# Optimization experiments

Measured on AMD Instinct MI355X. Metric: run time of the kernel, lower is better.

Reference implementation:

```python
import jax, jax.numpy as jnp
import numpy as np
import math

DIM = 1024
MAX_DEPTH = 16
ROPE_BASE = 10000.0
NUM_ACTIVE = 2

def setup_inputs() -> dict:
    key = jax.random.key(0)
    ks = jax.random.split(key, 6)
    bsz, seq, dim, E, hidden = 4, 1024, DIM, 8, 4 * DIM
    bound = 1.0 / math.sqrt(dim)
    return {
        "x": jax.random.normal(ks[0], (bsz, seq, dim), jnp.float32),
        "router_w": jax.random.normal(ks[1], (dim, dim), jnp.float32) * 0.02,
        "expert_keys": jax.random.uniform(ks[2], (E, dim), jnp.float32, -bound, bound),
        "expert_bias": jnp.zeros((E,), jnp.float32),
        "fc_w": jax.random.normal(ks[3], (E, hidden, dim), jnp.float32) * 0.02,
        "proj_w": jax.random.normal(ks[4], (E, dim, hidden), jnp.float32) * 0.02,
        "depth_idx": 3,
    }

def _rope_row(depth_idx, rev_idx, dtype):
    half = DIM // 2
    inv_freq = 1.0 / (ROPE_BASE ** (jnp.arange(0, DIM, 2, dtype=jnp.float32) / DIM))  # [half]
    f = depth_idx * inv_freq
    r = rev_idx * inv_freq
    return (jnp.cos(f).astype(dtype), jnp.sin(f).astype(dtype),
            jnp.cos(r).astype(dtype), jnp.sin(r).astype(dtype))

def reference(x, router_w, expert_keys, expert_bias, fc_w, proj_w, depth_idx):
    bsz, seq, dim = x.shape
    N = bsz * seq
    flat_x = x.reshape(N, dim)
    # router + RMSNorm (no weight, eps = machine eps, matching F.rms_norm default)
    q = flat_x @ router_w.T
    eps = jnp.asarray(jnp.finfo(q.dtype).eps, q.dtype)
    q = q * jax.lax.rsqrt(jnp.mean(q * q, axis=-1, keepdims=True) + eps)
    # depth RoPE (forward freq on first half pairing, reverse freq on second half)
    half = dim // 2
    cos, sin, rcos, rsin = _rope_row(float(depth_idx), float(MAX_DEPTH - 1 - depth_idx), q.dtype)
    q1, q2 = q[..., :half], q[..., half:]
    q = jnp.concatenate((q1 * cos + q2 * sin, -q1 * rsin + q2 * rcos), axis=-1)
    # routing
    logits = (q @ expert_keys.T) / math.sqrt(dim)  # [N, E]
    gate_values = jax.nn.sigmoid(logits)
    biased = logits + expert_bias
    _, topk_idx = jax.lax.top_k(biased, NUM_ACTIVE)  # [N, k]
    topk_gates = jnp.take_along_axis(gate_values, topk_idx, axis=-1)
    topk_gates = topk_gates / jnp.clip(topk_gates.sum(-1, keepdims=True), 1e-9, None)
    gates = jnp.zeros_like(gate_values).at[jnp.arange(N)[:, None], topk_idx].set(topk_gates)
    # dense all-expert MLP: relu(x W_fc^T)^2 W_proj^T, then mask-and-sum
    h = jax.nn.relu(jnp.einsum('nd,ehd->neh', flat_x, fc_w))
    expert_out = jnp.einsum('neh,edh->ned', h * h, proj_w)  # [N, E, dim]
    y = jnp.einsum('ned,ne->nd', expert_out, gates)
    return y.reshape(bsz, seq, dim)
```

## Files before the change

kernel.cpp:

```cpp
#include <hip/hip_runtime.h>
#include <hip/hip_bf16.h>
#include <math.h>

#define N_TOK 4096
#define DIM_V 1024
#define NEXP  8
#define HID   4096
#define NSLOT 9216

typedef short  s16x8 __attribute__((ext_vector_type(8)));
typedef unsigned short u16x8 __attribute__((ext_vector_type(8)));
typedef unsigned short u16x4 __attribute__((ext_vector_type(4)));
typedef float  f32x4 __attribute__((ext_vector_type(4)));

constexpr size_t OFF_XB   = 0;
constexpr size_t OFF_WB   = OFF_XB + 8388608;
constexpr size_t OFF_RK   = OFF_WB + 2097152;
constexpr size_t OFF_KPP  = OFF_RK + 65536;
constexpr size_t OFF_SSQ  = OFF_KPP + 65536;
constexpr size_t OFF_CNT  = OFF_SSQ + 16384;
constexpr size_t OFF_CUR  = OFF_CNT + 128;
constexpr size_t OFF_TOK  = OFF_CUR + 128;
constexpr size_t OFF_GSL  = OFF_TOK + 36864;
constexpr size_t ZERO_BEG = OFF_KPP;
constexpr size_t ZERO_END = OFF_GSL + 36864;
constexpr size_t OFF_OFFP = ZERO_END;
constexpr size_t OFF_IDX2 = OFF_OFFP + 128;
constexpr size_t OFF_G2   = OFF_IDX2 + 32768;
constexpr size_t OFF_INV  = OFF_G2 + 32768;
constexpr size_t SMALL_END = OFF_INV + 32768;

constexpr size_t A_OFF_FCB = SMALL_END;
constexpr size_t A_OFF_PO  = A_OFF_FCB;
constexpr size_t A_OFF_PJB = A_OFF_FCB + 67108864;
constexpr size_t A_OFF_H2  = A_OFF_PJB + 67108864;
constexpr size_t WS_FULL   = A_OFF_H2 + 75497472;

__device__ inline unsigned short f2bf(float f) {
  __hip_bfloat16 h = __float2bfloat16(f);
  return __builtin_bit_cast(unsigned short, h);
}

__device__ __forceinline__ void gload16(const void* g, void* l) {
  __builtin_amdgcn_global_load_lds(
      (const __attribute__((address_space(1))) unsigned int*)g,
      (__attribute__((address_space(3))) unsigned int*)l, 16, 0, 0);
}

__global__ __launch_bounds__(256) void k_cvt_all(
    const float* __restrict__ x, const float* __restrict__ rw,
    const float* __restrict__ fw, const float* __restrict__ pw,
    unsigned short* __restrict__ xb, unsigned short* __restrict__ wb,
    unsigned short* __restrict__ fcb, unsigned short* __restrict__ pjb) {
  constexpr int NX4 = (N_TOK * DIM_V) / 4;
  constexpr int NW4 = (DIM_V * DIM_V) / 4;
  constexpr int NF4 = (NEXP * HID * DIM_V) / 4;
  constexpr int NU  = (NX4 + NW4 + 2 * NF4) / 1024;
  const int upb = (NU + (int)gridDim.x - 1) / (int)gridDim.x;
  for (int k = 0; k < upb; ++k) {
    int u = (int)blockIdx.x * upb + k;
    if (u >= NU) break;
    int f4 = u * 1024;
    const float4* s; unsigned short* d; int base;
    if (f4 < NX4)                   { s = (const float4*)x;  d = xb;  base = f4; }
    else if (f4 < NX4 + NW4)        { s = (const float4*)rw; d = wb;  base = f4 - NX4; }
    else if (f4 < NX4 + NW4 + NF4)  { s = (const float4*)fw; d = fcb; base = f4 - NX4 - NW4; }
    else                            { s = (const float4*)pw; d = pjb; base = f4 - NX4 - NW4 - NF4; }
    int j = base + (int)threadIdx.x;
    const f32x4* s4 = (const f32x4*)s;
    f32x4 v0 = __builtin_nontemporal_load(s4 + j);
    f32x4 v1 = __builtin_nontemporal_load(s4 + j + 256);
    f32x4 v2 = __builtin_nontemporal_load(s4 + j + 512);
    f32x4 v3 = __builtin_nontemporal_load(s4 + j + 768);
    u16x4 o0 = { f2bf(v0.x), f2bf(v0.y), f2bf(v0.z), f2bf(v0.w) };
    u16x4 o1 = { f2bf(v1.x), f2bf(v1.y), f2bf(v1.z), f2bf(v1.w) };
    u16x4 o2 = { f2bf(v2.x), f2bf(v2.y), f2bf(v2.z), f2bf(v2.w) };
    u16x4 o3 = { f2bf(v3.x), f2bf(v3.y), f2bf(v3.z), f2bf(v3.w) };
    __builtin_nontemporal_store(o0, (u16x4*)(d + (size_t)j * 4));
    __builtin_nontemporal_store(o1, (u16x4*)(d + (size_t)(j + 256) * 4));
    __builtin_nontemporal_store(o2, (u16x4*)(d + (size_t)(j + 512) * 4));
    __builtin_nontemporal_store(o3, (u16x4*)(d + (size_t)(j + 768) * 4));
  }
}

__global__ void k_ropekeys(const float* __restrict__ keys, const int* __restrict__ depth,
                           double* __restrict__ rk) {
  int i = threadIdx.x;
  if (i >= 512) return;
  int dep = depth[0];
  double p = pow(10000.0, (double)i / 512.0);
  float invf = 1.0f / (float)p;
  float ff = (float)dep * invf;
  float rr = (float)(15 - dep) * invf;
  float cf  = (float)cos((double)ff);
  float sf  = (float)sin((double)ff);
  float rcf = (float)cos((double)rr);
  float rsf = (float)sin((double)rr);
  for (int e = 0; e < NEXP; ++e) {
    double k1 = (double)keys[e * DIM_V + i];
    double k2 = (double)keys[e * DIM_V + 512 + i];
    rk[e * DIM_V + i]       = (double)cf  * k1 - (double)rsf * k2;
    rk[e * DIM_V + 512 + i] = (double)sf  * k1 + (double)rcf * k2;
  }
}

__global__ __launch_bounds__(256) void k_colsum(const float* __restrict__ W,
                                                const double* __restrict__ rk,
                                                double* __restrict__ kpp) {
  int j  = blockIdx.x * 256 + threadIdx.x;
  int d0 = blockIdx.y * 64;
  double acc[NEXP] = {};
  for (int dd = 0; dd < 64; ++dd) {
    int d = d0 + dd;
    double w = (double)W[(size_t)d * DIM_V + j];
#pragma unroll
    for (int e = 0; e < NEXP; ++e) acc[e] += w * rk[e * DIM_V + d];
  }
  for (int e = 0; e < NEXP; ++e) atomicAdd(&kpp[e * DIM_V + j], acc[e]);
}

__global__ __launch_bounds__(256) void k_gate(const float* __restrict__ x,
                                              const double* __restrict__ kpp,
                                              const float* __restrict__ sumsq,
                                              const float* __restrict__ bias,
                                              int* __restrict__ idx2, float* __restrict__ gates2,
                                              int* __restrict__ counts) {
  int wave = (blockIdx.x * 256 + threadIdx.x) >> 6;
  int lane = threadIdx.x & 63;
  if (wave >= N_TOK) return;
  const float4* xr = (const float4*)(x + (size_t)wave * DIM_V);
  double a[NEXP] = {};
#pragma unroll
  for (int j = 0; j < 4; ++j) {
    int c = lane + 64 * j;
    float4 v = xr[c];
#pragma unroll
    for (int e = 0; e < NEXP; ++e) {
      const double* kp = kpp + (size_t)e * DIM_V + c * 4;
      a[e] += (double)v.x * kp[0] + (double)v.y * kp[1] +
              (double)v.z * kp[2] + (double)v.w * kp[3];
    }
  }
#pragma unroll
  for (int e = 0; e < NEXP; ++e)
    for (int d = 1; d < 64; d <<= 1) a[e] += __shfl_xor(a[e], d, 64);
  if (lane == 0) {
    float s = rsqrtf(sumsq[wave] * (1.0f / 1024.0f) + 1.1920928955078125e-7f);
    float z[NEXP], b[NEXP];
#pragma unroll
    for (int e = 0; e < NEXP; ++e) {
      z[e] = (float)(a[e] * (double)s * (1.0 / 32.0));
      b[e] = z[e] + bias[e];
    }
    int i1 = 0;
    for (int e = 1; e < NEXP; ++e) if (b[e] > b[i1]) i1 = e;
    int i2 = -1;
    for (int e = 0; e < NEXP; ++e) if (e != i1 && (i2 < 0 || b[e] > b[i2])) i2 = e;
    float g1 = 1.f / (1.f + expf(-z[i1]));
    float g2 = 1.f / (1.f + expf(-z[i2]));
    float sm = fmaxf(g1 + g2, 1e-9f);
    idx2[wave * 2] = i1; idx2[wave * 2 + 1] = i2;
    gates2[wave * 2] = g1 / sm; gates2[wave * 2 + 1] = g2 / sm;
    atomicAdd(&counts[i1], 1); atomicAdd(&counts[i2], 1);
  }
}

__global__ void k_scatter(const int* __restrict__ idx2, const float* __restrict__ gates2,
                          const int* __restrict__ counts, int* __restrict__ cursor,
                          int* __restrict__ tok, float* __restrict__ gsl,
                          int* __restrict__ inv, int* __restrict__ offp_out) {
  int off[NEXP + 1];
  off[0] = 0;
  for (int e = 0; e < NEXP; ++e) off[e + 1] = off[e] + ((counts[e] + 127) & ~127);
  int n = blockIdx.x * 256 + threadIdx.x;
  if (blockIdx.x == 0 && threadIdx.x == 0)
    for (int e = 0; e <= NEXP; ++e) offp_out[e] = off[e];
  if (n >= N_TOK) return;
  for (int r = 0; r < 2; ++r) {
    int e = idx2[n * 2 + r];
    int pos = atomicAdd(&cursor[e], 1);
    int slot = off[e] + pos;
    tok[slot] = n; gsl[slot] = gates2[n * 2 + r]; inv[n * 2 + r] = slot;
  }
}

__global__ __launch_bounds__(512) void k_fc256(
    const unsigned short* __restrict__ xb,
    const unsigned short* __restrict__ fcb,
    const int* __restrict__ offp, const int* __restrict__ tok,
    unsigned short* __restrict__ h2) {
  constexpr int KD = DIM_V;
  constexpr int NT = KD / 64;
  const int G = gridDim.x, q = G >> 3;
  const int idp = ((int)blockIdx.x & 7) * q + ((int)blockIdx.x >> 3);
  const int bx = idp >> 4;
  const int n0 = (idp & 15) * 256;
  int c = 0, e = 0, m0 = -1;
  for (e = 0; e < NEXP; ++e) {
    int nb = (offp[e + 1] - offp[e] + 255) >> 8;
    if (bx < c + nb) { m0 = offp[e] + (bx - c) * 256; break; }
    c += nb;
  }
  if (m0 < 0) return;
  const int segend = offp[e + 1];
  const unsigned short* Bp = fcb + ((size_t)e * HID + n0) * KD;

  __shared__ alignas(16) char smem[131072];
  const int tid = threadIdx.x, wid = tid >> 6, lane = tid & 63;
  const int wr = (wid >> 2) * 128, wcc = (wid & 3) * 64;
  const int swc8 = ((tid & 7) ^ ((tid >> 3) & 7)) * 8;
  const int frow = lane & 15, fsl = lane >> 4, fkey = lane & 7;

  int arow[4];
#pragma unroll
  for (int p = 0; p < 4; ++p) {
    int rr = m0 + p * 64 + (tid >> 3);
    arow[p] = tok[rr < NSLOT ? rr : NSLOT - 1];
  }

  auto stage = [&](int k0s, unsigned db) {
#pragma unroll
    for (int p = 0; p < 4; ++p)
      gload16(xb + (size_t)arow[p] * KD + k0s + swc8,
              smem + db + p * 8192 + wid * 1024);
#pragma unroll
    for (int p = 0; p < 4; ++p)
      gload16(Bp + (size_t)(p * 64 + (tid >> 3)) * KD + k0s + swc8,
              smem + db + 32768 + p * 8192 + wid * 1024);
  };

  f32x4 acc[8][4] = {};
  stage(0, 0);
  for (int t = 0; t < NT; ++t) {
    int tn = t + 1; if (tn == NT) tn = 0;
    stage(tn * 64, (unsigned)((t + 1) & 1) * 65536u);
    asm volatile("s_waitcnt vmcnt(8)" ::: "memory");
    __builtin_amdgcn_s_barrier();
    __builtin_amdgcn_sched_barrier(0);
    const unsigned Ab = (unsigned)(t & 1) * 65536u, Bb = Ab + 32768u;
#pragma unroll
    for (int kk2 = 0; kk2 < 2; ++kk2) {
      const unsigned so = (unsigned)(((fsl + kk2 * 4) ^ fkey) << 4);
      s16x8 af[8], bfr[4];
#pragma unroll
      for (int m = 0; m < 8; ++m)
        af[m] = *(const s16x8*)(smem + Ab + (unsigned)(wr + m * 16 + frow) * 128 + so);
#pragma unroll
      for (int n = 0; n < 4; ++n)
        bfr[n] = *(const s16x8*)(smem + Bb + (unsigned)(wcc + n * 16 + frow) * 128 + so);
      __builtin_amdgcn_s_setprio(1);
#pragma unroll
      for (int m = 0; m < 8; ++m)
#pragma unroll
        for (int n = 0; n < 4; ++n)
          acc[m][n] = __builtin_amdgcn_mfma_f32_16x16x32_bf16(af[m], bfr[n], acc[m][n], 0, 0, 0);
      __builtin_amdgcn_s_setprio(0);
    }
    __builtin_amdgcn_sched_barrier(0);
    __builtin_amdgcn_s_barrier();
  }
#pragma unroll
  for (int m = 0; m < 8; ++m)
#pragma unroll
    for (int j = 0; j < 4; ++j) {
      const int grow = m0 + wr + m * 16 + (lane >> 4) * 4 + j;
      if (grow < segend) {
#pragma unroll
        for (int n = 0; n < 4; ++n) {
          float v = acc[m][n][j];
          v = v > 0.f ? v * v : 0.f;
          h2[(size_t)grow * HID + n0 + wcc + n * 16 + (lane & 15)] = f2bf(v);
        }
      }
    }
}

__global__ __launch_bounds__(256) void k_proj2(
    const unsigned short* __restrict__ h2,
    const unsigned short* __restrict__ pjb,
    const int* __restrict__ offp, const float* __restrict__ gsl,
    float* __restrict__ po) {
  constexpr int KD  = HID;
  constexpr int KS  = KD / 2;
  constexpr int NT  = KS / 64;
  constexpr int GNB = DIM_V / 128;
  const int G = gridDim.x, q = G >> 3;
  const int idp = ((int)blockIdx.x & 7) * q + ((int)blockIdx.x >> 3);
  const int n0 = (idp % GNB) * 128;
  const int mi = (idp / GNB) % (NSLOT / 128);
  const int ks = idp / (GNB * (NSLOT / 128));
  const int m0 = mi * 128;
  if (m0 >= offp[NEXP]) return;
  int e = 0; while (e < NEXP - 1 && m0 >= offp[e + 1]) ++e;
  const unsigned short* Bp = pjb + ((size_t)e * DIM_V + n0) * KD + ks * KS;
  const unsigned short* Ap = h2 + ks * KS;

  __shared__ alignas(16) char smem[65536];
  const int tid = threadIdx.x, wid = tid >> 6, lane = tid & 63;
  const int wr = (wid >> 1) * 64, wc = (wid & 1) * 64;
  const int rql  = tid >> 3;
  const int swc8 = ((tid & 7) ^ ((tid >> 3) & 7)) * 8;
  const int frow = lane & 15, fsl = lane >> 4, fkey = lane & 7;

  auto stage = [&](int k0s, unsigned db) {
#pragma unroll
    for (int p = 0; p < 4; ++p)
      gload16(Ap + (size_t)(m0 + p * 32 + rql) * KD + k0s + swc8,
              smem + db + p * 4096 + wid * 1024);
#pragma unroll
    for (int p = 0; p < 4; ++p)
      gload16(Bp + (size_t)(p * 32 + rql) * KD + k0s + swc8,
              smem + db + 16384 + p * 4096 + wid * 1024);
  };

  f32x4 acc[4][4] = {};
  stage(0, 0);
#pragma unroll 2
  for (int t = 0; t < NT; ++t) {
    int tn = t + 1; if (tn == NT) tn = 0;
    stage(tn * 64, (unsigned)((t + 1) & 1) * 32768u);
    asm volatile("s_waitcnt vmcnt(8)" ::: "memory");
    __builtin_amdgcn_s_barrier();
    __builtin_amdgcn_sched_barrier(0);
    const unsigned Ab = (unsigned)(t & 1) * 32768u, Bb = Ab + 16384u;
    s16x8 af[2][4], bfr[2][4];
#pragma unroll
    for (int kk2 = 0; kk2 < 2; ++kk2) {
      const unsigned so = (unsigned)(((fsl + kk2 * 4) ^ fkey) << 4);
#pragma unroll
      for (int m = 0; m < 4; ++m)
        af[kk2][m] = *(const s16x8*)(smem + Ab + (unsigned)(wr + m * 16 + frow) * 128 + so);
#pragma unroll
      for (int n = 0; n < 4; ++n)
        bfr[kk2][n] = *(const s16x8*)(smem + Bb + (unsigned)(wc + n * 16 + frow) * 128 + so);
    }
    __builtin_amdgcn_s_setprio(1);
#pragma unroll
    for (int kk2 = 0; kk2 < 2; ++kk2)
#pragma unroll
      for (int m = 0; m < 4; ++m)
#pragma unroll
        for (int n = 0; n < 4; ++n)
          acc[m][n] = __builtin_amdgcn_mfma_f32_16x16x32_bf16(af[kk2][m], bfr[kk2][n],
                                                              acc[m][n], 0, 0, 0);
    __builtin_amdgcn_s_setprio(0);
    __builtin_amdgcn_sched_barrier(0);
    __builtin_amdgcn_s_barrier();
  }

#pragma unroll
  for (int m = 0; m < 4; ++m)
#pragma unroll
    for (int j = 0; j < 4; ++j) {
      const int grow = m0 + wr + m * 16 + (lane >> 4) * 4 + j;
      const float g = gsl[grow];
#pragma unroll
      for (int n = 0; n < 4; ++n)
        atomicAdd(&po[(size_t)grow * DIM_V + n0 + wc + n * 16 + (lane & 15)],
                  acc[m][n][j] * g);
    }
}

__global__ __launch_bounds__(256) void k_qt(
    const unsigned short* __restrict__ Aptr,
    const unsigned short* __restrict__ Wptr,
    float* __restrict__ sumsq) {
  constexpr int KD = DIM_V;
  constexpr int GNB = DIM_V / 128;
  constexpr int NT  = KD / 64;
  const int G = gridDim.x, q = G >> 3;
  const int idp = ((int)blockIdx.x & 7) * q + ((int)blockIdx.x >> 3);
  const int n0 = (idp % GNB) * 128, m0 = (idp / GNB) * 128;
  const unsigned short* Bp = Wptr + (size_t)n0 * KD;

  __shared__ alignas(16) char smem[65536];
  const int tid = threadIdx.x, wid = tid >> 6, lane = tid & 63;
  const int wr = (wid >> 1) * 64, wc = (wid & 1) * 64;
  const int rql  = tid >> 3;
  const int swc8 = ((tid & 7) ^ ((tid >> 3) & 7)) * 8;
  const int frow = lane & 15, fsl = lane >> 4, fkey = lane & 7;

  auto stage = [&](int k0s, unsigned db) {
#pragma unroll
    for (int p = 0; p < 4; ++p)
      gload16(Aptr + (size_t)(m0 + p * 32 + rql) * KD + k0s + swc8,
              smem + db + p * 4096 + wid * 1024);
#pragma unroll
    for (int p = 0; p < 4; ++p)
      gload16(Bp + (size_t)(p * 32 + rql) * KD + k0s + swc8,
              smem + db + 16384 + p * 4096 + wid * 1024);
  };

  f32x4 acc[4][4] = {};
  stage(0, 0);
#pragma unroll 2
  for (int t = 0; t < NT; ++t) {
    int tn = t + 1; if (tn == NT) tn = 0;
    stage(tn * 64, (unsigned)((t + 1) & 1) * 32768u);
    asm volatile("s_waitcnt vmcnt(8)" ::: "memory");
    __builtin_amdgcn_s_barrier();
    __builtin_amdgcn_sched_barrier(0);
    const unsigned Ab = (unsigned)(t & 1) * 32768u, Bb = Ab + 16384u;
    s16x8 af[2][4], bfr[2][4];
#pragma unroll
    for (int kk2 = 0; kk2 < 2; ++kk2) {
      const unsigned so = (unsigned)(((fsl + kk2 * 4) ^ fkey) << 4);
#pragma unroll
      for (int m = 0; m < 4; ++m)
        af[kk2][m] = *(const s16x8*)(smem + Ab + (unsigned)(wr + m * 16 + frow) * 128 + so);
#pragma unroll
      for (int n = 0; n < 4; ++n)
        bfr[kk2][n] = *(const s16x8*)(smem + Bb + (unsigned)(wc + n * 16 + frow) * 128 + so);
    }
    __builtin_amdgcn_s_setprio(1);
#pragma unroll
    for (int kk2 = 0; kk2 < 2; ++kk2)
#pragma unroll
      for (int m = 0; m < 4; ++m)
#pragma unroll
        for (int n = 0; n < 4; ++n)
          acc[m][n] = __builtin_amdgcn_mfma_f32_16x16x32_bf16(af[kk2][m], bfr[kk2][n],
                                                              acc[m][n], 0, 0, 0);
    __builtin_amdgcn_s_setprio(0);
    __builtin_amdgcn_sched_barrier(0);
    __builtin_amdgcn_s_barrier();
  }

#pragma unroll
  for (int m = 0; m < 4; ++m)
#pragma unroll
    for (int j = 0; j < 4; ++j) {
      const int grow = m0 + wr + m * 16 + (lane >> 4) * 4 + j;
      float s = 0.f;
#pragma unroll
      for (int n = 0; n < 4; ++n) { float v = acc[m][n][j]; s += v * v; }
      s += __shfl_xor(s, 1, 64); s += __shfl_xor(s, 2, 64);
      s += __shfl_xor(s, 4, 64); s += __shfl_xor(s, 8, 64);
      if ((lane & 15) == 0) atomicAdd(&sumsq[grow], s);
    }
}

__global__ void k_combine(const float* __restrict__ po, const int* __restrict__ inv,
                          float* __restrict__ y) {
  const int total = N_TOK * (DIM_V / 4);
  for (int i = blockIdx.x * blockDim.x + threadIdx.x; i < total;
       i += gridDim.x * blockDim.x) {
    int n = i >> 8, c = i & 255;
    int s1 = inv[n * 2], s2 = inv[n * 2 + 1];
    float4 a = ((const float4*)(po + (size_t)s1 * DIM_V))[c];
    float4 b = ((const float4*)(po + (size_t)s2 * DIM_V))[c];
    float4 o; o.x = a.x + b.x; o.y = a.y + b.y; o.z = a.z + b.z; o.w = a.w + b.w;
    ((float4*)(y + (size_t)n * DIM_V))[c] = o;
  }
}

extern "C" void kernel_launch(void* const* d_in, const int* in_sizes, int n_in,
                              void* d_out, int out_size, void* d_ws, size_t ws_size,
                              hipStream_t stream) {
  if (ws_size < WS_FULL) return;
  const float* x      = (const float*)d_in[0];
  const float* rw     = (const float*)d_in[1];
  const float* keys   = (const float*)d_in[2];
  const float* bias   = (const float*)d_in[3];
  const float* fc_w   = (const float*)d_in[4];
  const float* proj_w = (const float*)d_in[5];
  const int*   depth  = (const int*)d_in[6];
  char* ws = (char*)d_ws;
  unsigned short* xb  = (unsigned short*)(ws + OFF_XB);
  unsigned short* wb  = (unsigned short*)(ws + OFF_WB);
  double* rk    = (double*)(ws + OFF_RK);
  double* kpp   = (double*)(ws + OFF_KPP);
  float*  ssq   = (float*)(ws + OFF_SSQ);
  int*    cnt   = (int*)(ws + OFF_CNT);
  int*    cur   = (int*)(ws + OFF_CUR);
  int*    tok   = (int*)(ws + OFF_TOK);
  float*  gsl   = (float*)(ws + OFF_GSL);
  int*    offp  = (int*)(ws + OFF_OFFP);
  int*    idx2  = (int*)(ws + OFF_IDX2);
  float*  g2    = (float*)(ws + OFF_G2);
  int*    inv   = (int*)(ws + OFF_INV);
  unsigned short* fcb = (unsigned short*)(ws + A_OFF_FCB);
  unsigned short* pjb = (unsigned short*)(ws + A_OFF_PJB);
  unsigned short* h2  = (unsigned short*)(ws + A_OFF_H2);
  float*  po    = (float*)(ws + A_OFF_PO);
  float*  y     = (float*)d_out;

  hipMemsetAsync(ws + ZERO_BEG, 0, ZERO_END - ZERO_BEG, stream);
  k_cvt_all<<<2208, 256, 0, stream>>>(x, rw, fc_w, proj_w, xb, wb, fcb, pjb);
  k_ropekeys<<<1, 512, 0, stream>>>(keys, depth, rk);
  k_colsum<<<dim3(4, 16), 256, 0, stream>>>(rw, rk, kpp);
  k_qt<<<dim3(32 * 8), 256, 0, stream>>>(xb, wb, ssq);
  k_gate<<<1024, 256, 0, stream>>>(x, kpp, ssq, bias, idx2, g2, cnt);
  k_scatter<<<16, 256, 0, stream>>>(idx2, g2, cnt, cur, tok, gsl, inv, offp);
  k_fc256<<<dim3(44 * 16), 512, 0, stream>>>(xb, fcb, offp, tok, h2);
  hipMemsetAsync(po, 0, (size_t)NSLOT * DIM_V * 4, stream);
  k_proj2<<<dim3(72 * 8 * 2), 256, 0, stream>>>(h2, pjb, offp, gsl, po);
  k_combine<<<2048, 256, 0, stream>>>(po, inv, y);
}
```

Baseline: 491.0 us.

## Fuse expert projection with combine via atomic scatter into output

Projection GEMM no longer splits K in two. Its gated results are atomically added straight into the output row of each token, found through the slot-to-token map. This drops the large per-slot intermediate buffer, the memset that cleared it and the separate combine kernel; only the output is zeroed now. The cost is half as many blocks with twice the K loop each, plus atomic contention when a token's two experts write the same output row. Padded slots may also feed uninitialised h2 values into token 0 through a zero gate, which would turn any NaN there into NaN output.

```diff
diff --git a/kernel.cpp b/kernel.cpp
--- a/kernel.cpp
+++ b/kernel.cpp
@@ -31,7 +31,6 @@
 constexpr size_t SMALL_END = OFF_INV + 32768;
 
 constexpr size_t A_OFF_FCB = SMALL_END;
-constexpr size_t A_OFF_PO  = A_OFF_FCB;
 constexpr size_t A_OFF_PJB = A_OFF_FCB + 67108864;
 constexpr size_t A_OFF_H2  = A_OFF_PJB + 67108864;
 constexpr size_t WS_FULL   = A_OFF_H2 + 75497472;
@@ -184,6 +183,85 @@
   }
 }
 
+__global__ __launch_bounds__(256) void k_qt(
+    const unsigned short* __restrict__ Aptr,
+    const unsigned short* __restrict__ Wptr,
+    float* __restrict__ sumsq) {
+  constexpr int KD = DIM_V;
+  constexpr int GNB = DIM_V / 128;
+  constexpr int NT  = KD / 64;
+  const int G = gridDim.x, q = G >> 3;
+  const int idp = ((int)blockIdx.x & 7) * q + ((int)blockIdx.x >> 3);
+  const int n0 = (idp % GNB) * 128, m0 = (idp / GNB) * 128;
+  const unsigned short* Bp = Wptr + (size_t)n0 * KD;
+
+  __shared__ alignas(16) char smem[65536];
+  const int tid = threadIdx.x, wid = tid >> 6, lane = tid & 63;
+  const int wr = (wid >> 1) * 64, wc = (wid & 1) * 64;
+  const int rql  = tid >> 3;
+  const int swc8 = ((tid & 7) ^ ((tid >> 3) & 7)) * 8;
+  const int frow = lane & 15, fsl = lane >> 4, fkey = lane & 7;
+
+  auto stage = [&](int k0s, unsigned db) {
+#pragma unroll
+    for (int p = 0; p < 4; ++p)
+      gload16(Aptr + (size_t)(m0 + p * 32 + rql) * KD + k0s + swc8,
+              smem + db + p * 4096 + wid * 1024);
+#pragma unroll
+    for (int p = 0; p < 4; ++p)
+      gload16(Bp + (size_t)(p * 32 + rql) * KD + k0s + swc8,
+              smem + db + 16384 + p * 4096 + wid * 1024);
+  };
+
+  f32x4 acc[4][4] = {};
+  stage(0, 0);
+#pragma unroll 2
+  for (int t = 0; t < NT; ++t) {
+    int tn = t + 1; if (tn == NT) tn = 0;
+    stage(tn * 64, (unsigned)((t + 1) & 1) * 32768u);
+    asm volatile("s_waitcnt vmcnt(8)" ::: "memory");
+    __builtin_amdgcn_s_barrier();
+    __builtin_amdgcn_sched_barrier(0);
+    const unsigned Ab = (unsigned)(t & 1) * 32768u, Bb = Ab + 16384u;
+    s16x8 af[2][4], bfr[2][4];
+#pragma unroll
+    for (int kk2 = 0; kk2 < 2; ++kk2) {
+      const unsigned so = (unsigned)(((fsl + kk2 * 4) ^ fkey) << 4);
+#pragma unroll
+      for (int m = 0; m < 4; ++m)
+        af[kk2][m] = *(const s16x8*)(smem + Ab + (unsigned)(wr + m * 16 + frow) * 128 + so);
+#pragma unroll
+      for (int n = 0; n < 4; ++n)
+        bfr[kk2][n] = *(const s16x8*)(smem + Bb + (unsigned)(wc + n * 16 + frow) * 128 + so);
+    }
+    __builtin_amdgcn_s_setprio(1);
+#pragma unroll
+    for (int kk2 = 0; kk2 < 2; ++kk2)
+#pragma unroll
+      for (int m = 0; m < 4; ++m)
+#pragma unroll
+        for (int n = 0; n < 4; ++n)
+          acc[m][n] = __builtin_amdgcn_mfma_f32_16x16x32_bf16(af[kk2][m], bfr[kk2][n],
+                                                              acc[m][n], 0, 0, 0);
+    __builtin_amdgcn_s_setprio(0);
+    __builtin_amdgcn_sched_barrier(0);
+    __builtin_amdgcn_s_barrier();
+  }
+
+#pragma unroll
+  for (int m = 0; m < 4; ++m)
+#pragma unroll
+    for (int j = 0; j < 4; ++j) {
+      const int grow = m0 + wr + m * 16 + (lane >> 4) * 4 + j;
+      float s = 0.f;
+#pragma unroll
+      for (int n = 0; n < 4; ++n) { float v = acc[m][n][j]; s += v * v; }
+      s += __shfl_xor(s, 1, 64); s += __shfl_xor(s, 2, 64);
+      s += __shfl_xor(s, 4, 64); s += __shfl_xor(s, 8, 64);
+      if ((lane & 15) == 0) atomicAdd(&sumsq[grow], s);
+    }
+}
+
 __global__ __launch_bounds__(512) void k_fc256(
     const unsigned short* __restrict__ xb,
     const unsigned short* __restrict__ fcb,
@@ -275,25 +353,20 @@
     }
 }
 
-__global__ __launch_bounds__(256) void k_proj2(
+__global__ __launch_bounds__(256) void k_projy(
     const unsigned short* __restrict__ h2,
     const unsigned short* __restrict__ pjb,
-    const int* __restrict__ offp, const float* __restrict__ gsl,
-    float* __restrict__ po) {
+    const int* __restrict__ offp, const int* __restrict__ tok,
+    const float* __restrict__ gsl, float* __restrict__ y) {
   constexpr int KD  = HID;
-  constexpr int KS  = KD / 2;
-  constexpr int NT  = KS / 64;
   constexpr int GNB = DIM_V / 128;
+  constexpr int NT  = KD / 64;
   const int G = gridDim.x, q = G >> 3;
   const int idp = ((int)blockIdx.x & 7) * q + ((int)blockIdx.x >> 3);
-  const int n0 = (idp % GNB) * 128;
-  const int mi = (idp / GNB) % (NSLOT / 128);
-  const int ks = idp / (GNB * (NSLOT / 128));
-  const int m0 = mi * 128;
+  const int n0 = (idp % GNB) * 128, m0 = (idp / GNB) * 128;
   if (m0 >= offp[NEXP]) return;
   int e = 0; while (e < NEXP - 1 && m0 >= offp[e + 1]) ++e;
-  const unsigned short* Bp = pjb + ((size_t)e * DIM_V + n0) * KD + ks * KS;
-  const unsigned short* Ap = h2 + ks * KS;
+  const unsigned short* Bp = pjb + ((size_t)e * DIM_V + n0) * KD;
 
   __shared__ alignas(16) char smem[65536];
   const int tid = threadIdx.x, wid = tid >> 6, lane = tid & 63;
@@ -305,7 +378,7 @@
   auto stage = [&](int k0s, unsigned db) {
 #pragma unroll
     for (int p = 0; p < 4; ++p)
-      gload16(Ap + (size_t)(m0 + p * 32 + rql) * KD + k0s + swc8,
+      gload16(h2 + (size_t)(m0 + p * 32 + rql) * KD + k0s + swc8,
               smem + db + p * 4096 + wid * 1024);
 #pragma unroll
     for (int p = 0; p < 4; ++p)
@@ -354,104 +427,12 @@
     for (int j = 0; j < 4; ++j) {
       const int grow = m0 + wr + m * 16 + (lane >> 4) * 4 + j;
       const float g = gsl[grow];
+      const int token = tok[grow];
+      float* yr = y + (size_t)token * DIM_V + n0 + wc + (lane & 15);
 #pragma unroll
       for (int n = 0; n < 4; ++n)
-        atomicAdd(&po[(size_t)grow * DIM_V + n0 + wc + n * 16 + (lane & 15)],
-                  acc[m][n][j] * g);
-    }
-}
-
-__global__ __launch_bounds__(256) void k_qt(
-    const unsigned short* __restrict__ Aptr,
-    const unsigned short* __restrict__ Wptr,
-    float* __restrict__ sumsq) {
-  constexpr int KD = DIM_V;
-  constexpr int GNB = DIM_V / 128;
-  constexpr int NT  = KD / 64;
-  const int G = gridDim.x, q = G >> 3;
-  const int idp = ((int)blockIdx.x & 7) * q + ((int)blockIdx.x >> 3);
-  const int n0 = (idp % GNB) * 128, m0 = (idp / GNB) * 128;
-  const unsigned short* Bp = Wptr + (size_t)n0 * KD;
-
-  __shared__ alignas(16) char smem[65536];
-  const int tid = threadIdx.x, wid = tid >> 6, lane = tid & 63;
-  const int wr = (wid >> 1) * 64, wc = (wid & 1) * 64;
-  const int rql  = tid >> 3;
-  const int swc8 = ((tid & 7) ^ ((tid >> 3) & 7)) * 8;
-  const int frow = lane & 15, fsl = lane >> 4, fkey = lane & 7;
-
-  auto stage = [&](int k0s, unsigned db) {
-#pragma unroll
-    for (int p = 0; p < 4; ++p)
-      gload16(Aptr + (size_t)(m0 + p * 32 + rql) * KD + k0s + swc8,
-              smem + db + p * 4096 + wid * 1024);
-#pragma unroll
-    for (int p = 0; p < 4; ++p)
-      gload16(Bp + (size_t)(p * 32 + rql) * KD + k0s + swc8,
-              smem + db + 16384 + p * 4096 + wid * 1024);
-  };
-
-  f32x4 acc[4][4] = {};
-  stage(0, 0);
-#pragma unroll 2
-  for (int t = 0; t < NT; ++t) {
-    int tn = t + 1; if (tn == NT) tn = 0;
-    stage(tn * 64, (unsigned)((t + 1) & 1) * 32768u);
-    asm volatile("s_waitcnt vmcnt(8)" ::: "memory");
-    __builtin_amdgcn_s_barrier();
-    __builtin_amdgcn_sched_barrier(0);
-    const unsigned Ab = (unsigned)(t & 1) * 32768u, Bb = Ab + 16384u;
-    s16x8 af[2][4], bfr[2][4];
-#pragma unroll
-    for (int kk2 = 0; kk2 < 2; ++kk2) {
-      const unsigned so = (unsigned)(((fsl + kk2 * 4) ^ fkey) << 4);
-#pragma unroll
-      for (int m = 0; m < 4; ++m)
-        af[kk2][m] = *(const s16x8*)(smem + Ab + (unsigned)(wr + m * 16 + frow) * 128 + so);
-#pragma unroll
-      for (int n = 0; n < 4; ++n)
-        bfr[kk2][n] = *(const s16x8*)(smem + Bb + (unsigned)(wc + n * 16 + frow) * 128 + so);
-    }
-    __builtin_amdgcn_s_setprio(1);
-#pragma unroll
-    for (int kk2 = 0; kk2 < 2; ++kk2)
-#pragma unroll
-      for (int m = 0; m < 4; ++m)
-#pragma unroll
-        for (int n = 0; n < 4; ++n)
-          acc[m][n] = __builtin_amdgcn_mfma_f32_16x16x32_bf16(af[kk2][m], bfr[kk2][n],
-                                                              acc[m][n], 0, 0, 0);
-    __builtin_amdgcn_s_setprio(0);
-    __builtin_amdgcn_sched_barrier(0);
-    __builtin_amdgcn_s_barrier();
-  }
-
-#pragma unroll
-  for (int m = 0; m < 4; ++m)
-#pragma unroll
-    for (int j = 0; j < 4; ++j) {
-      const int grow = m0 + wr + m * 16 + (lane >> 4) * 4 + j;
-      float s = 0.f;
-#pragma unroll
-      for (int n = 0; n < 4; ++n) { float v = acc[m][n][j]; s += v * v; }
-      s += __shfl_xor(s, 1, 64); s += __shfl_xor(s, 2, 64);
-      s += __shfl_xor(s, 4, 64); s += __shfl_xor(s, 8, 64);
-      if ((lane & 15) == 0) atomicAdd(&sumsq[grow], s);
-    }
-}
-
-__global__ void k_combine(const float* __restrict__ po, const int* __restrict__ inv,
-                          float* __restrict__ y) {
-  const int total = N_TOK * (DIM_V / 4);
-  for (int i = blockIdx.x * blockDim.x + threadIdx.x; i < total;
-       i += gridDim.x * blockDim.x) {
-    int n = i >> 8, c = i & 255;
-    int s1 = inv[n * 2], s2 = inv[n * 2 + 1];
-    float4 a = ((const float4*)(po + (size_t)s1 * DIM_V))[c];
-    float4 b = ((const float4*)(po + (size_t)s2 * DIM_V))[c];
-    float4 o; o.x = a.x + b.x; o.y = a.y + b.y; o.z = a.z + b.z; o.w = a.w + b.w;
-    ((float4*)(y + (size_t)n * DIM_V))[c] = o;
-  }
+        atomicAdd(&yr[n * 16], acc[m][n][j] * g);
+    }
 }
 
 extern "C" void kernel_launch(void* const* d_in, const int* in_sizes, int n_in,
@@ -482,10 +463,10 @@
   unsigned short* fcb = (unsigned short*)(ws + A_OFF_FCB);
   unsigned short* pjb = (unsigned short*)(ws + A_OFF_PJB);
   unsigned short* h2  = (unsigned short*)(ws + A_OFF_H2);
-  float*  po    = (float*)(ws + A_OFF_PO);
   float*  y     = (float*)d_out;
 
   hipMemsetAsync(ws + ZERO_BEG, 0, ZERO_END - ZERO_BEG, stream);
+  hipMemsetAsync(d_out, 0, (size_t)out_size * sizeof(float), stream);
   k_cvt_all<<<2208, 256, 0, stream>>>(x, rw, fc_w, proj_w, xb, wb, fcb, pjb);
   k_ropekeys<<<1, 512, 0, stream>>>(keys, depth, rk);
   k_colsum<<<dim3(4, 16), 256, 0, stream>>>(rw, rk, kpp);
@@ -493,7 +474,5 @@
   k_gate<<<1024, 256, 0, stream>>>(x, kpp, ssq, bias, idx2, g2, cnt);
   k_scatter<<<16, 256, 0, stream>>>(idx2, g2, cnt, cur, tok, gsl, inv, offp);
   k_fc256<<<dim3(44 * 16), 512, 0, stream>>>(xb, fcb, offp, tok, h2);
-  hipMemsetAsync(po, 0, (size_t)NSLOT * DIM_V * 4, stream);
-  k_proj2<<<dim3(72 * 8 * 2), 256, 0, stream>>>(h2, pjb, offp, gsl, po);
-  k_combine<<<2048, 256, 0, stream>>>(po, inv, y);
-}
+  k_projy<<<dim3(72 * 8), 256, 0, stream>>>(h2, pjb, offp, tok, gsl, y);
+}
```

Measured after the change: 520.3 us. 1.06x slower.

## Drop split-K atomics in proj GEMM, fold rope keys into colsum, streamline cvt

Applied to the files above, without the earlier changes.

The projection GEMM no longer splits K in two. Each block now covers the full hidden dimension and writes gated results with plain stores. This removes the 37 MB memset of the partial-output buffer and the float atomicAdds, at the cost of half as many blocks and longer per-block K loops. The separate single-block rope-keys kernel is fused into the column-sum kernel, which computes its 64 rotated key rows into shared memory. The conversion kernel now processes fixed contiguous chunks of 8 units per block, with an inner loop per source region.

```diff
diff --git a/kernel.cpp b/kernel.cpp
--- a/kernel.cpp
+++ b/kernel.cpp
@@ -52,69 +52,74 @@
     const float* __restrict__ fw, const float* __restrict__ pw,
     unsigned short* __restrict__ xb, unsigned short* __restrict__ wb,
     unsigned short* __restrict__ fcb, unsigned short* __restrict__ pjb) {
-  constexpr int NX4 = (N_TOK * DIM_V) / 4;
-  constexpr int NW4 = (DIM_V * DIM_V) / 4;
-  constexpr int NF4 = (NEXP * HID * DIM_V) / 4;
-  constexpr int NU  = (NX4 + NW4 + 2 * NF4) / 1024;
-  const int upb = (NU + (int)gridDim.x - 1) / (int)gridDim.x;
-  for (int k = 0; k < upb; ++k) {
-    int u = (int)blockIdx.x * upb + k;
-    if (u >= NU) break;
-    int f4 = u * 1024;
-    const float4* s; unsigned short* d; int base;
-    if (f4 < NX4)                   { s = (const float4*)x;  d = xb;  base = f4; }
-    else if (f4 < NX4 + NW4)        { s = (const float4*)rw; d = wb;  base = f4 - NX4; }
-    else if (f4 < NX4 + NW4 + NF4)  { s = (const float4*)fw; d = fcb; base = f4 - NX4 - NW4; }
-    else                            { s = (const float4*)pw; d = pjb; base = f4 - NX4 - NW4 - NF4; }
-    int j = base + (int)threadIdx.x;
-    const f32x4* s4 = (const f32x4*)s;
-    f32x4 v0 = __builtin_nontemporal_load(s4 + j);
-    f32x4 v1 = __builtin_nontemporal_load(s4 + j + 256);
-    f32x4 v2 = __builtin_nontemporal_load(s4 + j + 512);
-    f32x4 v3 = __builtin_nontemporal_load(s4 + j + 768);
-    u16x4 o0 = { f2bf(v0.x), f2bf(v0.y), f2bf(v0.z), f2bf(v0.w) };
-    u16x4 o1 = { f2bf(v1.x), f2bf(v1.y), f2bf(v1.z), f2bf(v1.w) };
-    u16x4 o2 = { f2bf(v2.x), f2bf(v2.y), f2bf(v2.z), f2bf(v2.w) };
-    u16x4 o3 = { f2bf(v3.x), f2bf(v3.y), f2bf(v3.z), f2bf(v3.w) };
-    __builtin_nontemporal_store(o0, (u16x4*)(d + (size_t)j * 4));
-    __builtin_nontemporal_store(o1, (u16x4*)(d + (size_t)(j + 256) * 4));
-    __builtin_nontemporal_store(o2, (u16x4*)(d + (size_t)(j + 512) * 4));
-    __builtin_nontemporal_store(o3, (u16x4*)(d + (size_t)(j + 768) * 4));
-  }
-}
-
-__global__ void k_ropekeys(const float* __restrict__ keys, const int* __restrict__ depth,
-                           double* __restrict__ rk) {
-  int i = threadIdx.x;
-  if (i >= 512) return;
-  int dep = depth[0];
-  double p = pow(10000.0, (double)i / 512.0);
-  float invf = 1.0f / (float)p;
-  float ff = (float)dep * invf;
-  float rr = (float)(15 - dep) * invf;
-  float cf  = (float)cos((double)ff);
-  float sf  = (float)sin((double)ff);
-  float rcf = (float)cos((double)rr);
-  float rsf = (float)sin((double)rr);
-  for (int e = 0; e < NEXP; ++e) {
-    double k1 = (double)keys[e * DIM_V + i];
-    double k2 = (double)keys[e * DIM_V + 512 + i];
-    rk[e * DIM_V + i]       = (double)cf  * k1 - (double)rsf * k2;
-    rk[e * DIM_V + 512 + i] = (double)sf  * k1 + (double)rcf * k2;
+  constexpr int E0 = (N_TOK * DIM_V) / 4096;
+  constexpr int E1 = E0 + (DIM_V * DIM_V) / 4096;
+  constexpr int E2 = E1 + (NEXP * HID * DIM_V) / 4096;
+  constexpr int E3 = E2 + (NEXP * HID * DIM_V) / 4096;
+  constexpr int UPB = 8;
+  int u = (int)blockIdx.x * UPB;
+  const int uend = u + UPB;
+  while (u < uend) {
+    const f32x4* s; u16x4* d; int ru0, rend;
+    if (u < E0)      { s = (const f32x4*)x;  d = (u16x4*)xb;  ru0 = 0;  rend = E0; }
+    else if (u < E1) { s = (const f32x4*)rw; d = (u16x4*)wb;  ru0 = E0; rend = E1; }
+    else if (u < E2) { s = (const f32x4*)fw; d = (u16x4*)fcb; ru0 = E1; rend = E2; }
+    else             { s = (const f32x4*)pw; d = (u16x4*)pjb; ru0 = E2; rend = E3; }
+    const int span = (uend < rend ? uend : rend) - u;
+    int j = (u - ru0) * 1024 + (int)threadIdx.x;
+#pragma unroll 2
+    for (int k = 0; k < span; ++k, j += 1024) {
+      f32x4 v0 = __builtin_nontemporal_load(s + j);
+      f32x4 v1 = __builtin_nontemporal_load(s + j + 256);
+      f32x4 v2 = __builtin_nontemporal_load(s + j + 512);
+      f32x4 v3 = __builtin_nontemporal_load(s + j + 768);
+      u16x4 o0 = { f2bf(v0.x), f2bf(v0.y), f2bf(v0.z), f2bf(v0.w) };
+      u16x4 o1 = { f2bf(v1.x), f2bf(v1.y), f2bf(v1.z), f2bf(v1.w) };
+      u16x4 o2 = { f2bf(v2.x), f2bf(v2.y), f2bf(v2.z), f2bf(v2.w) };
+      u16x4 o3 = { f2bf(v3.x), f2bf(v3.y), f2bf(v3.z), f2bf(v3.w) };
+      __builtin_nontemporal_store(o0, d + j);
+      __builtin_nontemporal_store(o1, d + j + 256);
+      __builtin_nontemporal_store(o2, d + j + 512);
+      __builtin_nontemporal_store(o3, d + j + 768);
+    }
+    u += span;
   }
 }
 
 __global__ __launch_bounds__(256) void k_colsum(const float* __restrict__ W,
-                                                const double* __restrict__ rk,
+                                                const float* __restrict__ keys,
+                                                const int* __restrict__ depth,
                                                 double* __restrict__ kpp) {
-  int j  = blockIdx.x * 256 + threadIdx.x;
-  int d0 = blockIdx.y * 64;
+  __shared__ double rks[NEXP][64];
+  const int d0 = blockIdx.y * 64;
+  const int t = threadIdx.x;
+  if (t < 64) {
+    const int d = d0 + t;
+    const int dep = depth[0];
+    const bool lower = d < 512;
+    const int i = lower ? d : d - 512;
+    double p = pow(10000.0, (double)i / 512.0);
+    float invf = 1.0f / (float)p;
+    float ff = (float)dep * invf;
+    float rr = (float)(15 - dep) * invf;
+    float cf  = (float)cos((double)ff);
+    float sf  = (float)sin((double)ff);
+    float rcf = (float)cos((double)rr);
+    float rsf = (float)sin((double)rr);
+    for (int e = 0; e < NEXP; ++e) {
+      double k1 = (double)keys[e * DIM_V + i];
+      double k2 = (double)keys[e * DIM_V + 512 + i];
+      rks[e][t] = lower ? ((double)cf * k1 - (double)rsf * k2)
+                        : ((double)sf * k1 + (double)rcf * k2);
+    }
+  }
+  __syncthreads();
+  const int j = blockIdx.x * 256 + t;
   double acc[NEXP] = {};
   for (int dd = 0; dd < 64; ++dd) {
-    int d = d0 + dd;
-    double w = (double)W[(size_t)d * DIM_V + j];
-#pragma unroll
-    for (int e = 0; e < NEXP; ++e) acc[e] += w * rk[e * DIM_V + d];
+    double w = (double)W[(size_t)(d0 + dd) * DIM_V + j];
+#pragma unroll
+    for (int e = 0; e < NEXP; ++e) acc[e] += w * rks[e][dd];
   }
   for (int e = 0; e < NEXP; ++e) atomicAdd(&kpp[e * DIM_V + j], acc[e]);
 }
@@ -184,6 +189,85 @@
   }
 }
 
+__global__ __launch_bounds__(256) void k_qt(
+    const unsigned short* __restrict__ Aptr,
+    const unsigned short* __restrict__ Wptr,
+    float* __restrict__ sumsq) {
+  constexpr int KD = DIM_V;
+  constexpr int GNB = DIM_V / 128;
+  constexpr int NT  = KD / 64;
+  const int G = gridDim.x, q = G >> 3;
+  const int idp = ((int)blockIdx.x & 7) * q + ((int)blockIdx.x >> 3);
+  const int n0 = (idp % GNB) * 128, m0 = (idp / GNB) * 128;
+  const unsigned short* Bp = Wptr + (size_t)n0 * KD;
+
+  __shared__ alignas(16) char smem[65536];
+  const int tid = threadIdx.x, wid = tid >> 6, lane = tid & 63;
+  const int wr = (wid >> 1) * 64, wc = (wid & 1) * 64;
+  const int rql  = tid >> 3;
+  const int swc8 = ((tid & 7) ^ ((tid >> 3) & 7)) * 8;
+  const int frow = lane & 15, fsl = lane >> 4, fkey = lane & 7;
+
+  auto stage = [&](int k0s, unsigned db) {
+#pragma unroll
+    for (int p = 0; p < 4; ++p)
+      gload16(Aptr + (size_t)(m0 + p * 32 + rql) * KD + k0s + swc8,
+              smem + db + p * 4096 + wid * 1024);
+#pragma unroll
+    for (int p = 0; p < 4; ++p)
+      gload16(Bp + (size_t)(p * 32 + rql) * KD + k0s + swc8,
+              smem + db + 16384 + p * 4096 + wid * 1024);
+  };
+
+  f32x4 acc[4][4] = {};
+  stage(0, 0);
+#pragma unroll 2
+  for (int t = 0; t < NT; ++t) {
+    int tn = t + 1; if (tn == NT) tn = 0;
+    stage(tn * 64, (unsigned)((t + 1) & 1) * 32768u);
+    asm volatile("s_waitcnt vmcnt(8)" ::: "memory");
+    __builtin_amdgcn_s_barrier();
+    __builtin_amdgcn_sched_barrier(0);
+    const unsigned Ab = (unsigned)(t & 1) * 32768u, Bb = Ab + 16384u;
+    s16x8 af[2][4], bfr[2][4];
+#pragma unroll
+    for (int kk2 = 0; kk2 < 2; ++kk2) {
+      const unsigned so = (unsigned)(((fsl + kk2 * 4) ^ fkey) << 4);
+#pragma unroll
+      for (int m = 0; m < 4; ++m)
+        af[kk2][m] = *(const s16x8*)(smem + Ab + (unsigned)(wr + m * 16 + frow) * 128 + so);
+#pragma unroll
+      for (int n = 0; n < 4; ++n)
+        bfr[kk2][n] = *(const s16x8*)(smem + Bb + (unsigned)(wc + n * 16 + frow) * 128 + so);
+    }
+    __builtin_amdgcn_s_setprio(1);
+#pragma unroll
+    for (int kk2 = 0; kk2 < 2; ++kk2)
+#pragma unroll
+      for (int m = 0; m < 4; ++m)
+#pragma unroll
+        for (int n = 0; n < 4; ++n)
+          acc[m][n] = __builtin_amdgcn_mfma_f32_16x16x32_bf16(af[kk2][m], bfr[kk2][n],
+                                                              acc[m][n], 0, 0, 0);
+    __builtin_amdgcn_s_setprio(0);
+    __builtin_amdgcn_sched_barrier(0);
+    __builtin_amdgcn_s_barrier();
+  }
+
+#pragma unroll
+  for (int m = 0; m < 4; ++m)
+#pragma unroll
+    for (int j = 0; j < 4; ++j) {
+      const int grow = m0 + wr + m * 16 + (lane >> 4) * 4 + j;
+      float s = 0.f;
+#pragma unroll
+      for (int n = 0; n < 4; ++n) { float v = acc[m][n][j]; s += v * v; }
+      s += __shfl_xor(s, 1, 64); s += __shfl_xor(s, 2, 64);
+      s += __shfl_xor(s, 4, 64); s += __shfl_xor(s, 8, 64);
+      if ((lane & 15) == 0) atomicAdd(&sumsq[grow], s);
+    }
+}
+
 __global__ __launch_bounds__(512) void k_fc256(
     const unsigned short* __restrict__ xb,
     const unsigned short* __restrict__ fcb,
@@ -275,25 +359,20 @@
     }
 }
 
-__global__ __launch_bounds__(256) void k_proj2(
+__global__ __launch_bounds__(256) void k_proj(
     const unsigned short* __restrict__ h2,
     const unsigned short* __restrict__ pjb,
     const int* __restrict__ offp, const float* __restrict__ gsl,
     float* __restrict__ po) {
   constexpr int KD  = HID;
-  constexpr int KS  = KD / 2;
-  constexpr int NT  = KS / 64;
   constexpr int GNB = DIM_V / 128;
+  constexpr int NT  = KD / 64;
   const int G = gridDim.x, q = G >> 3;
   const int idp = ((int)blockIdx.x & 7) * q + ((int)blockIdx.x >> 3);
-  const int n0 = (idp % GNB) * 128;
-  const int mi = (idp / GNB) % (NSLOT / 128);
-  const int ks = idp / (GNB * (NSLOT / 128));
-  const int m0 = mi * 128;
+  const int n0 = (idp % GNB) * 128, m0 = (idp / GNB) * 128;
   if (m0 >= offp[NEXP]) return;
   int e = 0; while (e < NEXP - 1 && m0 >= offp[e + 1]) ++e;
-  const unsigned short* Bp = pjb + ((size_t)e * DIM_V + n0) * KD + ks * KS;
-  const unsigned short* Ap = h2 + ks * KS;
+  const unsigned short* Bp = pjb + ((size_t)e * DIM_V + n0) * KD;
 
   __shared__ alignas(16) char smem[65536];
   const int tid = threadIdx.x, wid = tid >> 6, lane = tid & 63;
@@ -305,7 +384,7 @@
   auto stage = [&](int k0s, unsigned db) {
 #pragma unroll
     for (int p = 0; p < 4; ++p)
-      gload16(Ap + (size_t)(m0 + p * 32 + rql) * KD + k0s + swc8,
+      gload16(h2 + (size_t)(m0 + p * 32 + rql) * KD + k0s + swc8,
               smem + db + p * 4096 + wid * 1024);
 #pragma unroll
     for (int p = 0; p < 4; ++p)
@@ -356,87 +435,7 @@
       const float g = gsl[grow];
 #pragma unroll
       for (int n = 0; n < 4; ++n)
-        atomicAdd(&po[(size_t)grow * DIM_V + n0 + wc + n * 16 + (lane & 15)],
-                  acc[m][n][j] * g);
-    }
-}
-
-__global__ __launch_bounds__(256) void k_qt(
-    const unsigned short* __restrict__ Aptr,
-    const unsigned short* __restrict__ Wptr,
-    float* __restrict__ sumsq) {
-  constexpr int KD = DIM_V;
-  constexpr int GNB = DIM_V / 128;
-  constexpr int NT  = KD / 64;
-  const int G = gridDim.x, q = G >> 3;
-  const int idp = ((int)blockIdx.x & 7) * q + ((int)blockIdx.x >> 3);
-  const int n0 = (idp % GNB) * 128, m0 = (idp / GNB) * 128;
-  const unsigned short* Bp = Wptr + (size_t)n0 * KD;
-
-  __shared__ alignas(16) char smem[65536];
-  const int tid = threadIdx.x, wid = tid >> 6, lane = tid & 63;
-  const int wr = (wid >> 1) * 64, wc = (wid & 1) * 64;
-  const int rql  = tid >> 3;
-  const int swc8 = ((tid & 7) ^ ((tid >> 3) & 7)) * 8;
-  const int frow = lane & 15, fsl = lane >> 4, fkey = lane & 7;
-
-  auto stage = [&](int k0s, unsigned db) {
-#pragma unroll
-    for (int p = 0; p < 4; ++p)
-      gload16(Aptr + (size_t)(m0 + p * 32 + rql) * KD + k0s + swc8,
-              smem + db + p * 4096 + wid * 1024);
-#pragma unroll
-    for (int p = 0; p < 4; ++p)
-      gload16(Bp + (size_t)(p * 32 + rql) * KD + k0s + swc8,
-              smem + db + 16384 + p * 4096 + wid * 1024);
-  };
-
-  f32x4 acc[4][4] = {};
-  stage(0, 0);
-#pragma unroll 2
-  for (int t = 0; t < NT; ++t) {
-    int tn = t + 1; if (tn == NT) tn = 0;
-    stage(tn * 64, (unsigned)((t + 1) & 1) * 32768u);
-    asm volatile("s_waitcnt vmcnt(8)" ::: "memory");
-    __builtin_amdgcn_s_barrier();
-    __builtin_amdgcn_sched_barrier(0);
-    const unsigned Ab = (unsigned)(t & 1) * 32768u, Bb = Ab + 16384u;
-    s16x8 af[2][4], bfr[2][4];
-#pragma unroll
-    for (int kk2 = 0; kk2 < 2; ++kk2) {
-      const unsigned so = (unsigned)(((fsl + kk2 * 4) ^ fkey) << 4);
-#pragma unroll
-      for (int m = 0; m < 4; ++m)
-        af[kk2][m] = *(const s16x8*)(smem + Ab + (unsigned)(wr + m * 16 + frow) * 128 + so);
-#pragma unroll
-      for (int n = 0; n < 4; ++n)
-        bfr[kk2][n] = *(const s16x8*)(smem + Bb + (unsigned)(wc + n * 16 + frow) * 128 + so);
-    }
-    __builtin_amdgcn_s_setprio(1);
-#pragma unroll
-    for (int kk2 = 0; kk2 < 2; ++kk2)
-#pragma unroll
-      for (int m = 0; m < 4; ++m)
-#pragma unroll
-        for (int n = 0; n < 4; ++n)
-          acc[m][n] = __builtin_amdgcn_mfma_f32_16x16x32_bf16(af[kk2][m], bfr[kk2][n],
-                                                              acc[m][n], 0, 0, 0);
-    __builtin_amdgcn_s_setprio(0);
-    __builtin_amdgcn_sched_barrier(0);
-    __builtin_amdgcn_s_barrier();
-  }
-
-#pragma unroll
-  for (int m = 0; m < 4; ++m)
-#pragma unroll
-    for (int j = 0; j < 4; ++j) {
-      const int grow = m0 + wr + m * 16 + (lane >> 4) * 4 + j;
-      float s = 0.f;
-#pragma unroll
-      for (int n = 0; n < 4; ++n) { float v = acc[m][n][j]; s += v * v; }
-      s += __shfl_xor(s, 1, 64); s += __shfl_xor(s, 2, 64);
-      s += __shfl_xor(s, 4, 64); s += __shfl_xor(s, 8, 64);
-      if ((lane & 15) == 0) atomicAdd(&sumsq[grow], s);
+        po[(size_t)grow * DIM_V + n0 + wc + n * 16 + (lane & 15)] = acc[m][n][j] * g;
     }
 }
 
@@ -468,7 +467,6 @@
   char* ws = (char*)d_ws;
   unsigned short* xb  = (unsigned short*)(ws + OFF_XB);
   unsigned short* wb  = (unsigned short*)(ws + OFF_WB);
-  double* rk    = (double*)(ws + OFF_RK);
   double* kpp   = (double*)(ws + OFF_KPP);
   float*  ssq   = (float*)(ws + OFF_SSQ);
   int*    cnt   = (int*)(ws + OFF_CNT);
@@ -487,13 +485,11 @@
 
   hipMemsetAsync(ws + ZERO_BEG, 0, ZERO_END - ZERO_BEG, stream);
   k_cvt_all<<<2208, 256, 0, stream>>>(x, rw, fc_w, proj_w, xb, wb, fcb, pjb);
-  k_ropekeys<<<1, 512, 0, stream>>>(keys, depth, rk);
-  k_colsum<<<dim3(4, 16), 256, 0, stream>>>(rw, rk, kpp);
+  k_colsum<<<dim3(4, 16), 256, 0, stream>>>(rw, keys, depth, kpp);
   k_qt<<<dim3(32 * 8), 256, 0, stream>>>(xb, wb, ssq);
   k_gate<<<1024, 256, 0, stream>>>(x, kpp, ssq, bias, idx2, g2, cnt);
   k_scatter<<<16, 256, 0, stream>>>(idx2, g2, cnt, cur, tok, gsl, inv, offp);
   k_fc256<<<dim3(44 * 16), 512, 0, stream>>>(xb, fcb, offp, tok, h2);
-  hipMemsetAsync(po, 0, (size_t)NSLOT * DIM_V * 4, stream);
-  k_proj2<<<dim3(72 * 8 * 2), 256, 0, stream>>>(h2, pjb, offp, gsl, po);
+  k_proj<<<dim3(72 * 8), 256, 0, stream>>>(h2, pjb, offp, gsl, po);
   k_combine<<<2048, 256, 0, stream>>>(po, inv, y);
 }
```

Measured after the change: 458.9 us. 6.5% less time.
